# Performance work log

Hardware: AMD Instinct MI355X
Metric: run time of the kernel (lower is better)

The kernel has to match this reference:

```python
import jax, jax.numpy as jnp
import numpy as np

N = 20000        # nodes
E = 320000       # edges (before self-loops)
NODE_F = 128
MSG_F = 256
LN_EPS = 1e-5


def _mlp2(x, w1, b1, w2, b2):
    return jax.nn.relu(x @ w1.T + b1) @ w2.T + b2


def _gatv2(x, src, dst, wl, wr, att, bias, heads, outc, concat, n):
    # PyG GATv2Conv (share_weights=False, negative_slope=0.2), eval mode (no dropout)
    xl = (x @ wl.T).reshape(n, heads, outc)   # source transform
    xr = (x @ wr.T).reshape(n, heads, outc)   # target transform
    e = jax.nn.leaky_relu(xl[src] + xr[dst], 0.2)          # [E, H, C]
    logits = jnp.einsum('ehc,hc->eh', e, att)              # [E, H]
    m = jax.ops.segment_max(logits, dst, num_segments=n)   # per-dst softmax max
    p = jnp.exp(logits - m[dst])
    denom = jax.ops.segment_sum(p, dst, num_segments=n)
    alpha = p / denom[dst]                                 # [E, H]
    out = jax.ops.segment_sum(alpha[:, :, None] * xl[src], dst, num_segments=n)
    out = out.reshape(n, heads * outc) if concat else out.mean(axis=1)
    return out + bias


def _forward(node_features, message_features, edge_index,
             me_w1, me_b1, me_w2, me_b2,
             ne_w1, ne_b1, ne_w2, ne_b2,
             c1_wl, c1_wr, c1_att, c1_b,
             c2_wl, c2_wr, c2_att, c2_b,
             c3_wl, c3_wr, c3_att, c3_b,
             en_w1, en_b1, en_w2, en_b2, ln_g, ln_b):
    n = node_features.shape[0]
    # PyG GATv2Conv add_self_loops=True by default
    ar = jnp.arange(n, dtype=edge_index.dtype)
    src = jnp.concatenate([edge_index[0], ar])
    dst = jnp.concatenate([edge_index[1], ar])

    msg_emb = _mlp2(message_features, me_w1, me_b1, me_w2, me_b2)   # [N,128]
    node_emb = _mlp2(node_features, ne_w1, ne_b1, ne_w2, ne_b2)     # [N,128]
    x = jnp.concatenate([node_emb, msg_emb], axis=1)                # [N,256]

    x = jax.nn.relu(_gatv2(x, src, dst, c1_wl, c1_wr, c1_att, c1_b, 4, 64, True, n))   # [N,256]
    x = jax.nn.relu(_gatv2(x, src, dst, c2_wl, c2_wr, c2_att, c2_b, 2, 64, True, n))   # [N,128]
    emb = _gatv2(x, src, dst, c3_wl, c3_wr, c3_att, c3_b, 1, 256, False, n)            # [N,256]

    h = _mlp2(emb, en_w1, en_b1, en_w2, en_b2)                      # [N,256]
    mu = h.mean(axis=-1, keepdims=True)
    var = ((h - mu) ** 2).mean(axis=-1, keepdims=True)
    return (h - mu) * jax.lax.rsqrt(var + LN_EPS) * ln_g + ln_b


def setup_inputs() -> dict:
    key = jax.random.key(0)
    ks = jax.random.split(key, 32)

    def w(k, shape):
        return jax.random.normal(k, shape, jnp.float32) / np.sqrt(shape[-1]).astype(np.float32)

    inp = {}
    inp['node_features'] = jax.random.normal(ks[0], (N, NODE_F), jnp.float32)
    inp['message_features'] = jax.random.normal(ks[1], (N, MSG_F), jnp.float32)
    inp['edge_index'] = jax.random.randint(ks[2], (2, E), 0, N, jnp.int32)
    # message encoder: msg->256->128
    inp['me_w1'] = w(ks[3], (256, MSG_F)); inp['me_b1'] = jnp.zeros((256,), jnp.float32)
    inp['me_w2'] = w(ks[4], (128, 256)); inp['me_b2'] = jnp.zeros((128,), jnp.float32)
    # node encoder: node->128->128
    inp['ne_w1'] = w(ks[5], (128, NODE_F)); inp['ne_b1'] = jnp.zeros((128,), jnp.float32)
    inp['ne_w2'] = w(ks[6], (128, 128)); inp['ne_b2'] = jnp.zeros((128,), jnp.float32)
    # conv1: 256 -> 4 heads x 64, concat
    inp['c1_wl'] = w(ks[7], (256, 256)); inp['c1_wr'] = w(ks[8], (256, 256))
    inp['c1_att'] = w(ks[9], (4, 64)); inp['c1_b'] = jnp.zeros((256,), jnp.float32)
    # conv2: 256 -> 2 heads x 64, concat
    inp['c2_wl'] = w(ks[10], (128, 256)); inp['c2_wr'] = w(ks[11], (128, 256))
    inp['c2_att'] = w(ks[12], (2, 64)); inp['c2_b'] = jnp.zeros((128,), jnp.float32)
    # conv3: 128 -> 1 head x 256, mean (concat=False)
    inp['c3_wl'] = w(ks[13], (256, 128)); inp['c3_wr'] = w(ks[14], (256, 128))
    inp['c3_att'] = w(ks[15], (1, 256)); inp['c3_b'] = jnp.zeros((256,), jnp.float32)
    # enhancer: 256->512->256 + LayerNorm
    inp['en_w1'] = w(ks[16], (512, 256)); inp['en_b1'] = jnp.zeros((512,), jnp.float32)
    inp['en_w2'] = w(ks[17], (256, 512)); inp['en_b2'] = jnp.zeros((256,), jnp.float32)
    inp['ln_g'] = jnp.ones((256,), jnp.float32); inp['ln_b'] = jnp.zeros((256,), jnp.float32)
    return inp


def reference(node_features, message_features, edge_index,
              me_w1, me_b1, me_w2, me_b2,
              ne_w1, ne_b1, ne_w2, ne_b2,
              c1_wl, c1_wr, c1_att, c1_b,
              c2_wl, c2_wr, c2_att, c2_b,
              c3_wl, c3_wr, c3_att, c3_b,
              en_w1, en_b1, en_w2, en_b2, ln_g, ln_b):
    return _forward(node_features, message_features, edge_index,
                    me_w1, me_b1, me_w2, me_b2,
                    ne_w1, ne_b1, ne_w2, ne_b2,
                    c1_wl, c1_wr, c1_att, c1_b,
                    c2_wl, c2_wr, c2_att, c2_b,
                    c3_wl, c3_wr, c3_att, c3_b,
                    en_w1, en_b1, en_w2, en_b2, ln_g, ln_b)
```

## Files before the change

### kernel.cpp

```cpp
#include <hip/hip_runtime.h>
#include <math.h>


static inline int ceildiv(int a, int b) { return (a + b - 1) / b; }

typedef _Float16 h8  __attribute__((ext_vector_type(8)));
typedef _Float16 h4v __attribute__((ext_vector_type(4)));
typedef _Float16 h2v __attribute__((ext_vector_type(2)));
typedef float    f4x __attribute__((ext_vector_type(4)));

__device__ __forceinline__ void gload16(const _Float16* g, _Float16* l) {
    __builtin_amdgcn_global_load_lds(
        (const __attribute__((address_space(1))) void*)g,
        (__attribute__((address_space(3))) void*)l, 16, 0, 0);
}

__global__ void fill_u32(unsigned int* __restrict__ p, int n, unsigned int v) {
    int i = blockIdx.x * blockDim.x + threadIdx.x;
    if (i < n) p[i] = v;
}

struct SplitArgs {
    const float* src[14];
    _Float16* dh[14];
    _Float16* dl[14];
    int off[15];
};

__global__ void split_multi(SplitArgs a, int totalv) {
    int v = blockIdx.x * blockDim.x + threadIdx.x;
    if (v >= totalv) return;
    int s = 0;
#pragma unroll
    for (int i = 1; i < 14; i++) s += (v >= a.off[i]);
    int lv = v - a.off[s];
    float4 f = ((const float4*)a.src[s])[lv];
    float vals[4] = {f.x, f.y, f.z, f.w};
    h4v hh, hl;
#pragma unroll
    for (int j = 0; j < 4; j++) {
        _Float16 h = (_Float16)vals[j];
        hh[j] = h;
        hl[j] = (_Float16)(vals[j] - (float)h);
    }
    *(h4v*)(a.dh[s] + (size_t)lv * 4) = hh;
    *(h4v*)(a.dl[s] + (size_t)lv * 4) = hl;
}

template <int OUT, bool RELU>
__global__ __launch_bounds__(256) void gemm_mfma(
    const _Float16* __restrict__ Ahi, const _Float16* __restrict__ Alo,
    const _Float16* __restrict__ Whi, const _Float16* __restrict__ Wlo,
    const float* __restrict__ bias, float* __restrict__ Cf,
    _Float16* __restrict__ Chi, _Float16* __restrict__ Clo,
    int M, int K, int ldc)
{
    __shared__ _Float16 sA[2][128][64];
    __shared__ _Float16 sW[2][64][64];
    const int t = threadIdx.x;
    const int lane = t & 63;
    const int w = t >> 6, wr = w >> 1, wc = w & 1;
    const int m0 = blockIdx.y * 128, n0 = blockIdx.x * 64;

    f4x acc[4][2] = {};

    for (int k0 = 0; k0 < K; k0 += 64) {
#pragma unroll
        for (int i = 0; i < 4; i++) {
            const int bv = w * 64 + i * 256;
            const int row = (bv >> 3) + (lane >> 3);
            const int c8 = (lane & 7) ^ (row & 7);
            int gr = m0 + row; if (gr > M - 1) gr = M - 1;
            const size_t g = (size_t)gr * K + k0 + c8 * 8;
            gload16(Ahi + g, &sA[0][0][0] + (size_t)bv * 8);
            gload16(Alo + g, &sA[1][0][0] + (size_t)bv * 8);
        }
#pragma unroll
        for (int i = 0; i < 2; i++) {
            const int bv = w * 64 + i * 256;
            const int row = (bv >> 3) + (lane >> 3);
            const int c8 = (lane & 7) ^ (row & 7);
            const size_t g = (size_t)(n0 + row) * K + k0 + c8 * 8;
            gload16(Whi + g, &sW[0][0][0] + (size_t)bv * 8);
            gload16(Wlo + g, &sW[1][0][0] + (size_t)bv * 8);
        }
        __syncthreads();
#pragma unroll
        for (int ks = 0; ks < 2; ks++) {
            const int kg = ks * 4 + (lane >> 4);
            h8 afh[4], afl[4], wfh[2], wfl[2];
#pragma unroll
            for (int mi = 0; mi < 4; mi++) {
                int row = wr * 64 + mi * 16 + (lane & 15);
                int cs = ((kg ^ (row & 7)) << 3);
                afh[mi] = *(const h8*)&sA[0][row][cs];
                afl[mi] = *(const h8*)&sA[1][row][cs];
            }
#pragma unroll
            for (int ni = 0; ni < 2; ni++) {
                int row = wc * 32 + ni * 16 + (lane & 15);
                int cs = ((kg ^ (row & 7)) << 3);
                wfh[ni] = *(const h8*)&sW[0][row][cs];
                wfl[ni] = *(const h8*)&sW[1][row][cs];
            }
#pragma unroll
            for (int mi = 0; mi < 4; mi++)
#pragma unroll
                for (int ni = 0; ni < 2; ni++) {
                    acc[mi][ni] = __builtin_amdgcn_mfma_f32_16x16x32_f16(
                        afh[mi], wfh[ni], acc[mi][ni], 0, 0, 0);
                    acc[mi][ni] = __builtin_amdgcn_mfma_f32_16x16x32_f16(
                        afh[mi], wfl[ni], acc[mi][ni], 0, 0, 0);
                    acc[mi][ni] = __builtin_amdgcn_mfma_f32_16x16x32_f16(
                        afl[mi], wfh[ni], acc[mi][ni], 0, 0, 0);
                }
        }
        __syncthreads();
    }
#pragma unroll
    for (int mi = 0; mi < 4; mi++) {
#pragma unroll
        for (int ni = 0; ni < 2; ni++) {
            int col = n0 + wc * 32 + ni * 16 + (lane & 15);
            float bz = bias ? bias[col] : 0.f;
#pragma unroll
            for (int r = 0; r < 4; r++) {
                int grow = m0 + wr * 64 + mi * 16 + (lane >> 4) * 4 + r;
                if (grow < M) {
                    float vv = acc[mi][ni][r] + bz;
                    if (RELU) vv = fmaxf(vv, 0.f);
                    if (OUT == 0) {
                        Cf[(size_t)grow * ldc + col] = vv;
                    } else if (OUT == 1) {
                        _Float16 h = (_Float16)vv;
                        Chi[(size_t)grow * ldc + col] = h;
                        Clo[(size_t)grow * ldc + col] = (_Float16)(vv - (float)h);
                    } else {
                        Chi[(size_t)grow * ldc + col] = (_Float16)vv;
                    }
                }
            }
        }
    }
}

__global__ void edge_count(const int* __restrict__ ei, int E, int ET,
                           int* __restrict__ cnt) {
    int e = blockIdx.x * blockDim.x + threadIdx.x;
    if (e >= ET) return;
    int dst = (e < E) ? ei[E + e] : e - E;
    atomicAdd(&cnt[dst], 1);
}

__global__ __launch_bounds__(1024) void scan_offsets(
    const int* __restrict__ cnt, int n, int* __restrict__ off,
    int* __restrict__ cur)
{
    __shared__ int s[1024];
    const int t = threadIdx.x;
    const int CH = (n + 1023) / 1024;
    int base = t * CH;
    int local[32];
    int sum = 0;
    for (int j = 0; j < CH; j++) {
        int idx = base + j;
        int v = (idx < n) ? cnt[idx] : 0;
        local[j] = sum;
        sum += v;
    }
    s[t] = sum;
    __syncthreads();
    for (int d = 1; d < 1024; d <<= 1) {
        int v = (t >= d) ? s[t - d] : 0;
        __syncthreads();
        s[t] += v;
        __syncthreads();
    }
    int excl = s[t] - sum;
    for (int j = 0; j < CH; j++) {
        int idx = base + j;
        if (idx < n) { off[idx] = excl + local[j]; cur[idx] = excl + local[j]; }
    }
    if (t == 1023) off[n] = s[1023];
}

__global__ void edge_scatter(const int* __restrict__ ei, int E, int ET,
                             int* __restrict__ cur, int* __restrict__ srcj) {
    int e = blockIdx.x * blockDim.x + threadIdx.x;
    if (e >= ET) return;
    int dst, src;
    if (e < E) { dst = ei[E + e]; src = ei[e]; } else { dst = src = e - E; }
    int pos = atomicAdd(&cur[dst], 1);
    srcj[pos] = src;
}

template <int H, int C, bool RELU>
__global__ __launch_bounds__(256) void gat_fused(
    const _Float16* __restrict__ xlr,
    const float* __restrict__ att, const float* __restrict__ bias,
    const int* __restrict__ srcj, const int* __restrict__ off, int Nn,
    _Float16* __restrict__ oh, _Float16* __restrict__ ol)
{
    constexpr int HC = H * C;
    constexpr int LD = 2 * HC;
    constexpr int R = HC / 64;
    constexpr int W2 = R / 2;
    constexpr int G = C / R;
    constexpr float L2E = 1.44269504088896f;
    constexpr float THR = 12.0f;
    const int wave = threadIdx.x >> 6;
    const int lane = threadIdx.x & 63;
    const int i = blockIdx.x * 4 + wave;
    if (i >= Nn) return;
    const int j0 = off[i], j1 = off[i + 1];

    h2v xr2[W2], at2[W2];
#pragma unroll
    for (int w2 = 0; w2 < W2; w2++) {
        int c = lane * R + 2 * w2;
        xr2[w2] = *(const h2v*)(xlr + (size_t)i * LD + HC + c);
        h2v a; a[0] = (_Float16)att[c]; a[1] = (_Float16)att[c + 1];
        at2[w2] = a;
    }

    float m2 = -INFINITY, sden = 0.f, acc[R] = {};

    auto LOADX = [&](int s, h2v* xv) {
        const _Float16* p = xlr + (size_t)s * LD + (size_t)lane * R;
        if constexpr (W2 == 2) {
            h4v hv = *(const h4v*)p;
            h2v a, b; a[0] = hv[0]; a[1] = hv[1]; b[0] = hv[2]; b[1] = hv[3];
            xv[0] = a; xv[1] = b;
        } else {
            xv[0] = *(const h2v*)p;
        }
    };

    h2v xv[W2];
    LOADX(srcj[j0], xv);
    for (int j = j0; j < j1; j++) {
        h2v xn[W2];
#pragma unroll
        for (int w2 = 0; w2 < W2; w2++) { h2v z = {0, 0}; xn[w2] = z; }
        if (j + 1 < j1) LOADX(srcj[j + 1], xn);

        float dot = 0.f;
#pragma unroll
        for (int w2 = 0; w2 < W2; w2++) {
            h2v v = xv[w2] + xr2[w2];
            h2v s5 = v * (_Float16)0.2f;
            h2v lk;
            lk[0] = v[0] > (_Float16)0 ? v[0] : s5[0];
            lk[1] = v[1] > (_Float16)0 ? v[1] : s5[1];
            dot = __builtin_amdgcn_fdot2(lk, at2[w2], dot, false);
        }
#pragma unroll
        for (int d = 1; d < G; d <<= 1) dot += __shfl_xor(dot, d);
        float l2 = dot * L2E;

        if (l2 - m2 > THR) {
            float sc = exp2f(m2 - l2);
            sden *= sc;
#pragma unroll
            for (int r = 0; r < R; r++) acc[r] *= sc;
            m2 = l2;
        }
        float p = exp2f(l2 - m2);
        sden += p;
#pragma unroll
        for (int w2 = 0; w2 < W2; w2++) {
            acc[2 * w2 + 0] += p * (float)xv[w2][0];
            acc[2 * w2 + 1] += p * (float)xv[w2][1];
        }
#pragma unroll
        for (int w2 = 0; w2 < W2; w2++) xv[w2] = xn[w2];
    }

    const float rd = 1.f / sden;
#pragma unroll
    for (int r = 0; r < R; r++) {
        int c = lane * R + r;
        float v = acc[r] * rd + bias[c];
        if (RELU) v = fmaxf(v, 0.f);
        _Float16 h = (_Float16)v;
        oh[(size_t)i * HC + c] = h;
        ol[(size_t)i * HC + c] = (_Float16)(v - (float)h);
    }
}

__global__ __launch_bounds__(256) void layernorm256(
    const float* __restrict__ x, const float* __restrict__ g,
    const float* __restrict__ b, float* __restrict__ out, int Nn)
{
    const int wave = threadIdx.x >> 6;
    const int lane = threadIdx.x & 63;
    const int i = blockIdx.x * 4 + wave;
    if (i >= Nn) return;
    float v[4];
    float sum = 0.f;
#pragma unroll
    for (int r = 0; r < 4; r++) {
        v[r] = x[(size_t)i * 256 + r * 64 + lane];
        sum += v[r];
    }
#pragma unroll
    for (int off = 32; off >= 1; off >>= 1) sum += __shfl_xor(sum, off);
    float mu = sum * (1.f / 256.f);
    float s2 = 0.f;
#pragma unroll
    for (int r = 0; r < 4; r++) { float d = v[r] - mu; s2 += d * d; }
#pragma unroll
    for (int off = 32; off >= 1; off >>= 1) s2 += __shfl_xor(s2, off);
    float rstd = 1.f / sqrtf(s2 * (1.f / 256.f) + 1e-5f);
#pragma unroll
    for (int r = 0; r < 4; r++) {
        int c = r * 64 + lane;
        out[(size_t)i * 256 + c] = (v[r] - mu) * rstd * g[c] + b[c];
    }
}

extern "C" void kernel_launch(void* const* d_in, const int* in_sizes, int n_in,
                              void* d_out, int out_size, void* d_ws,
                              size_t ws_size, hipStream_t stream)
{
    const float* node_f = (const float*)d_in[0];
    const float* msg_f  = (const float*)d_in[1];
    const int*   ei     = (const int*)d_in[2];
    const float* wsrc[12] = {
        (const float*)d_in[3],  (const float*)d_in[5],
        (const float*)d_in[7],  (const float*)d_in[9],
        (const float*)d_in[11], (const float*)d_in[12],
        (const float*)d_in[15], (const float*)d_in[16],
        (const float*)d_in[19], (const float*)d_in[20],
        (const float*)d_in[23], (const float*)d_in[25],
    };
    const int wsz[12] = {256*256, 128*256, 128*128, 128*128,
                         256*256, 256*256, 128*256, 128*256,
                         256*128, 256*128, 512*256, 256*512};
    const float* me_b1 = (const float*)d_in[4];
    const float* me_b2 = (const float*)d_in[6];
    const float* ne_b1 = (const float*)d_in[8];
    const float* ne_b2 = (const float*)d_in[10];
    const float* c1_at = (const float*)d_in[13];
    const float* c1_b  = (const float*)d_in[14];
    const float* c2_at = (const float*)d_in[17];
    const float* c2_b  = (const float*)d_in[18];
    const float* c3_at = (const float*)d_in[21];
    const float* c3_b  = (const float*)d_in[22];
    const float* en_b1 = (const float*)d_in[24];
    const float* en_b2 = (const float*)d_in[26];
    const float* ln_g  = (const float*)d_in[27];
    const float* ln_b  = (const float*)d_in[28];

    const int N  = in_sizes[0] / 128;
    const int E  = in_sizes[2] / 2;
    const int ET = E + N;

    char* base = (char*)d_ws;
    const size_t SZ = (size_t)N * 256 * 4;
    char* RA = base;
    char* RB = base + SZ;
    char* RC = base + 2 * SZ;
    char* RD = base + 3 * SZ;
    char* RE = base + 4 * SZ;
    char* RF = base + 5 * SZ;
    char* RG = base + 6 * SZ;

    _Float16* Pm_h = (_Float16*)RA;  _Float16* Pm_l = Pm_h + (size_t)N * 256;
    _Float16* X1_h = (_Float16*)RA;  _Float16* X1_l = X1_h + (size_t)N * 256;
    _Float16* Ph1_h = (_Float16*)RB; _Float16* Ph1_l = Ph1_h + (size_t)N * 256;
    _Float16* X3_h = (_Float16*)RB;  _Float16* X3_l = X3_h + (size_t)N * 256;
    float*    EN2  = (float*)RB;
    _Float16* Pn_h = (_Float16*)RC;  _Float16* Pn_l = Pn_h + (size_t)N * 128;
    _Float16* Pnh_h = Pn_l + (size_t)N * 128;
    _Float16* Pnh_l = Pnh_h + (size_t)N * 128;
    _Float16* X2_h = (_Float16*)RC;  _Float16* X2_l = X2_h + (size_t)N * 128;
    _Float16* X0_h = (_Float16*)RD;  _Float16* X0_l = X0_h + (size_t)N * 256;
    _Float16* XLR  = (_Float16*)RE;
    _Float16* HB_h = (_Float16*)RE;
    _Float16* HB_l = (_Float16*)RF;

    int* CNT = (int*)RG;
    int* OFF = CNT + N;
    int* CUR = OFF + N + 1;
    int* SRCJ = CUR + N;
    _Float16* WP = (_Float16*)(SRCJ + ET);

    _Float16 *wh[12], *wl[12];
    {
        _Float16* cur = WP;
        auto pair = [&](int i) { wh[i] = cur; cur += wsz[i]; wl[i] = cur; cur += wsz[i]; };
        pair(0); pair(1); pair(2); pair(3);
        auto stacked = [&](int i) {
            wh[i] = cur; wh[i+1] = cur + wsz[i]; cur += 2 * (size_t)wsz[i];
            wl[i] = cur; wl[i+1] = cur + wsz[i]; cur += 2 * (size_t)wsz[i];
        };
        stacked(4); stacked(6); stacked(8);
        pair(10); pair(11);
    }

    const dim3 B256(256);

    {
        SplitArgs sa;
        int cum = 0;
        for (int i = 0; i < 12; i++) {
            sa.src[i] = wsrc[i]; sa.dh[i] = wh[i]; sa.dl[i] = wl[i];
            sa.off[i] = cum; cum += wsz[i] / 4;
        }
        sa.src[12] = msg_f;  sa.dh[12] = Pm_h; sa.dl[12] = Pm_l;
        sa.off[12] = cum; cum += N * 256 / 4;
        sa.src[13] = node_f; sa.dh[13] = Pn_h; sa.dl[13] = Pn_l;
        sa.off[13] = cum; cum += N * 128 / 4;
        sa.off[14] = cum;
        split_multi<<<ceildiv(cum, 256), B256, 0, stream>>>(sa, cum);
    }

    fill_u32<<<ceildiv(N, 256), B256, 0, stream>>>((unsigned int*)CNT, N, 0u);
    edge_count<<<ceildiv(ET, 256), B256, 0, stream>>>(ei, E, ET, CNT);
    scan_offsets<<<1, 1024, 0, stream>>>(CNT, N, OFF, CUR);
    edge_scatter<<<ceildiv(ET, 256), B256, 0, stream>>>(ei, E, ET, CUR, SRCJ);

    const int MB_ = ceildiv(N, 128);
    const int GGAT = ceildiv(N, 4);

    gemm_mfma<1, true ><<<dim3(4, MB_), B256, 0, stream>>>(
        Pm_h, Pm_l, wh[0], wl[0], me_b1, nullptr, Ph1_h, Ph1_l, N, 256, 256);
    gemm_mfma<1, false><<<dim3(2, MB_), B256, 0, stream>>>(
        Ph1_h, Ph1_l, wh[1], wl[1], me_b2, nullptr, X0_h + 128, X0_l + 128, N, 256, 256);
    gemm_mfma<1, true ><<<dim3(2, MB_), B256, 0, stream>>>(
        Pn_h, Pn_l, wh[2], wl[2], ne_b1, nullptr, Pnh_h, Pnh_l, N, 128, 128);
    gemm_mfma<1, false><<<dim3(2, MB_), B256, 0, stream>>>(
        Pnh_h, Pnh_l, wh[3], wl[3], ne_b2, nullptr, X0_h, X0_l, N, 128, 256);

    gemm_mfma<2, false><<<dim3(8, MB_), B256, 0, stream>>>(
        X0_h, X0_l, wh[4], wl[4], nullptr, nullptr, XLR, nullptr, N, 256, 512);
    gat_fused<4, 64, true><<<GGAT, B256, 0, stream>>>(
        XLR, c1_at, c1_b, SRCJ, OFF, N, X1_h, X1_l);

    gemm_mfma<2, false><<<dim3(4, MB_), B256, 0, stream>>>(
        X1_h, X1_l, wh[6], wl[6], nullptr, nullptr, XLR, nullptr, N, 256, 256);
    gat_fused<2, 64, true><<<GGAT, B256, 0, stream>>>(
        XLR, c2_at, c2_b, SRCJ, OFF, N, X2_h, X2_l);

    gemm_mfma<2, false><<<dim3(8, MB_), B256, 0, stream>>>(
        X2_h, X2_l, wh[8], wl[8], nullptr, nullptr, XLR, nullptr, N, 128, 512);
    gat_fused<1, 256, false><<<GGAT, B256, 0, stream>>>(
        XLR, c3_at, c3_b, SRCJ, OFF, N, X3_h, X3_l);

    gemm_mfma<1, true ><<<dim3(8, MB_), B256, 0, stream>>>(
        X3_h, X3_l, wh[10], wl[10], en_b1, nullptr, HB_h, HB_l, N, 256, 512);
    gemm_mfma<0, false><<<dim3(4, MB_), B256, 0, stream>>>(
        HB_h, HB_l, wh[11], wl[11], en_b2, EN2, nullptr, nullptr, N, 512, 256);
    layernorm256<<<ceildiv(N, 4), B256, 0, stream>>>(EN2, ln_g, ln_b, (float*)d_out, N);
}
```

Measured before the change: 582.7 us.

## Process multiple edges per wave in GAT aggregation with 16-channel lane slices

The GATv2 aggregation kernel now assigns each lane a 16-channel slice, so one wave handles several edges at once (64/(HC/16) edges per iteration). Each edge group keeps its own online-softmax state, and the groups are merged at the end through xor-shuffle reductions that rescale by the running max. Loads become wide 16-byte vectors and the outputs are written as vectors. The aim is more edge-level parallelism and fewer serial iterations per node. In exchange, the software prefetch of the next edge is dropped, register use grows (16 accumulators), and the final merge adds cross-lane shuffle cost.

```diff
diff --git a/kernel.cpp b/kernel.cpp
--- a/kernel.cpp
+++ b/kernel.cpp
@@ -203,88 +203,107 @@
 {
     constexpr int HC = H * C;
     constexpr int LD = 2 * HC;
-    constexpr int R = HC / 64;
-    constexpr int W2 = R / 2;
-    constexpr int G = C / R;
+    constexpr int LPE = HC / 16;
+    constexpr int EPW = 64 / LPE;
+    constexpr int SUB = C / 16;
     constexpr float L2E = 1.44269504088896f;
     constexpr float THR = 12.0f;
     const int wave = threadIdx.x >> 6;
     const int lane = threadIdx.x & 63;
+    const int g = lane / LPE;
+    const int l = lane % LPE;
     const int i = blockIdx.x * 4 + wave;
     if (i >= Nn) return;
     const int j0 = off[i], j1 = off[i + 1];
 
-    h2v xr2[W2], at2[W2];
-#pragma unroll
-    for (int w2 = 0; w2 < W2; w2++) {
-        int c = lane * R + 2 * w2;
-        xr2[w2] = *(const h2v*)(xlr + (size_t)i * LD + HC + c);
+    h8 xr8[2];
+    xr8[0] = *(const h8*)(xlr + (size_t)i * LD + HC + l * 16);
+    xr8[1] = *(const h8*)(xlr + (size_t)i * LD + HC + l * 16 + 8);
+    const h2v* xr2 = (const h2v*)xr8;
+    h2v at2[8];
+#pragma unroll
+    for (int q = 0; q < 8; q++) {
+        int c = l * 16 + 2 * q;
         h2v a; a[0] = (_Float16)att[c]; a[1] = (_Float16)att[c + 1];
-        at2[w2] = a;
-    }
-
-    float m2 = -INFINITY, sden = 0.f, acc[R] = {};
-
-    auto LOADX = [&](int s, h2v* xv) {
-        const _Float16* p = xlr + (size_t)s * LD + (size_t)lane * R;
-        if constexpr (W2 == 2) {
-            h4v hv = *(const h4v*)p;
-            h2v a, b; a[0] = hv[0]; a[1] = hv[1]; b[0] = hv[2]; b[1] = hv[3];
-            xv[0] = a; xv[1] = b;
-        } else {
-            xv[0] = *(const h2v*)p;
-        }
-    };
-
-    h2v xv[W2];
-    LOADX(srcj[j0], xv);
-    for (int j = j0; j < j1; j++) {
-        h2v xn[W2];
-#pragma unroll
-        for (int w2 = 0; w2 < W2; w2++) { h2v z = {0, 0}; xn[w2] = z; }
-        if (j + 1 < j1) LOADX(srcj[j + 1], xn);
+        at2[q] = a;
+    }
+
+    float m2 = -INFINITY, sden = 0.f;
+    float acc[16] = {};
+
+    for (int jb = j0; jb < j1; jb += EPW) {
+        const int j = jb + g;
+        const bool valid = (j < j1);
+        const int jj = valid ? j : j1 - 1;
+        const int s = srcj[jj];
+        h8 xa[2];
+        const _Float16* xp = xlr + (size_t)s * LD + l * 16;
+        xa[0] = *(const h8*)xp;
+        xa[1] = *(const h8*)(xp + 8);
+        const h2v* xv2 = (const h2v*)xa;
 
         float dot = 0.f;
 #pragma unroll
-        for (int w2 = 0; w2 < W2; w2++) {
-            h2v v = xv[w2] + xr2[w2];
+        for (int q = 0; q < 8; q++) {
+            h2v v = xv2[q] + xr2[q];
             h2v s5 = v * (_Float16)0.2f;
             h2v lk;
             lk[0] = v[0] > (_Float16)0 ? v[0] : s5[0];
             lk[1] = v[1] > (_Float16)0 ? v[1] : s5[1];
-            dot = __builtin_amdgcn_fdot2(lk, at2[w2], dot, false);
-        }
-#pragma unroll
-        for (int d = 1; d < G; d <<= 1) dot += __shfl_xor(dot, d);
+            dot = __builtin_amdgcn_fdot2(lk, at2[q], dot, false);
+        }
+#pragma unroll
+        for (int d = 1; d < SUB; d <<= 1) dot += __shfl_xor(dot, d);
         float l2 = dot * L2E;
+        if (!valid) l2 = -1e30f;
 
         if (l2 - m2 > THR) {
             float sc = exp2f(m2 - l2);
             sden *= sc;
 #pragma unroll
-            for (int r = 0; r < R; r++) acc[r] *= sc;
+            for (int r = 0; r < 16; r++) acc[r] *= sc;
             m2 = l2;
         }
         float p = exp2f(l2 - m2);
         sden += p;
 #pragma unroll
-        for (int w2 = 0; w2 < W2; w2++) {
-            acc[2 * w2 + 0] += p * (float)xv[w2][0];
-            acc[2 * w2 + 1] += p * (float)xv[w2][1];
-        }
-#pragma unroll
-        for (int w2 = 0; w2 < W2; w2++) xv[w2] = xn[w2];
-    }
-
-    const float rd = 1.f / sden;
-#pragma unroll
-    for (int r = 0; r < R; r++) {
-        int c = lane * R + r;
-        float v = acc[r] * rd + bias[c];
-        if (RELU) v = fmaxf(v, 0.f);
-        _Float16 h = (_Float16)v;
-        oh[(size_t)i * HC + c] = h;
-        ol[(size_t)i * HC + c] = (_Float16)(v - (float)h);
+        for (int q = 0; q < 8; q++) {
+            acc[2 * q + 0] += p * (float)xv2[q][0];
+            acc[2 * q + 1] += p * (float)xv2[q][1];
+        }
+    }
+
+#pragma unroll
+    for (int d = LPE; d < 64; d <<= 1) {
+        float m2o = __shfl_xor(m2, d);
+        float sdo = __shfl_xor(sden, d);
+        float mn = fmaxf(m2, m2o);
+        float sa = exp2f(m2 - mn), sb = exp2f(m2o - mn);
+#pragma unroll
+        for (int r = 0; r < 16; r++) {
+            float ao = __shfl_xor(acc[r], d);
+            acc[r] = acc[r] * sa + ao * sb;
+        }
+        sden = sden * sa + sdo * sb;
+        m2 = mn;
+    }
+
+    if (g == 0) {
+        const float rd = 1.f / sden;
+        h8 vh[2], vl[2];
+#pragma unroll
+        for (int r = 0; r < 16; r++) {
+            int c = l * 16 + r;
+            float v = acc[r] * rd + bias[c];
+            if (RELU) v = fmaxf(v, 0.f);
+            _Float16 hh = (_Float16)v;
+            vh[r >> 3][r & 7] = hh;
+            vl[r >> 3][r & 7] = (_Float16)(v - (float)hh);
+        }
+        *(h8*)(oh + (size_t)i * HC + l * 16) = vh[0];
+        *(h8*)(oh + (size_t)i * HC + l * 16 + 8) = vh[1];
+        *(h8*)(ol + (size_t)i * HC + l * 16) = vl[0];
+        *(h8*)(ol + (size_t)i * HC + l * 16 + 8) = vl[1];
     }
 }
 
```

Measured after the change: 533.8 us. -8.4%, faster.
